# Performance work log

Hardware: AMD Instinct MI355X
Metric: run time of the kernel (lower is better)

## Reference

```python
import jax, jax.numpy as jnp
import numpy as np

N, D_IN, D_OUT, H = 8192, 512, 512, 8


def setup_inputs() -> dict:
    key = jax.random.key(0)
    k1, k2, k3, k4, k5 = jax.random.split(key, 5)
    x = jax.random.normal(k1, (N, D_IN), dtype=jnp.float32)
    adj = jax.random.randint(k2, (N, N), 0, 2, dtype=jnp.int32)
    W = jax.random.normal(k3, (D_OUT, D_IN), dtype=jnp.float32) * (1.0 / np.sqrt(D_IN))
    b = jax.random.normal(k4, (D_OUT,), dtype=jnp.float32) * 0.01
    a = jax.random.normal(k5, (H, 2 * (D_OUT // H)), dtype=jnp.float32)
    return {"x": x, "adj": adj, "W": W, "b": b, "a": a}


def reference(x, adj, W, b, a):
    # h = Linear(x): torch Linear stores W as [out, in]
    h = x @ W.T + b  # [N, D_OUT]
    # NOTE: the original forward computes dense GAT attention scores,
    # a masked softmax over adj, and an attention-weighted aggregation,
    # but then discards all of it and returns self.act(h). That attention
    # path is dead code (no effect on the output), so the faithful forward
    # is exactly GELU(Wx + b). torch.nn.GELU default is the exact erf form.
    return jax.nn.gelu(h, approximate=False)
```

## Files before the change

kernel.cpp:

```cpp
#include <hip/hip_runtime.h>
#include <hip/hip_bf16.h>
#include <math.h>


#define NROWS 8192
#define KD    512
#define NOUT  512

using short8  = __attribute__((ext_vector_type(8))) short;
using floatx4 = __attribute__((ext_vector_type(4))) float;

#define GLOBAL_AS(p) ((const __attribute__((address_space(1))) void*)(p))
#define LDS_AS(p)    ((__attribute__((address_space(3))) void*)(p))

__device__ __forceinline__ unsigned short f32_to_bf16(float f) {
  unsigned int u = __float_as_uint(f);
  u += 0x7FFFu + ((u >> 16) & 1u);
  return (unsigned short)(u >> 16);
}

__global__ __launch_bounds__(256) void cast_bf16_kernel(
    const float* __restrict__ x, const float* __restrict__ W,
    unsigned short* __restrict__ xb, unsigned short* __restrict__ wb) {
  const int i  = blockIdx.x * 256 + threadIdx.x;
  const int XV = (NROWS * KD) / 8;
  const float* src;
  unsigned short* dst;
  int idx;
  if (i < XV) { src = x; dst = xb; idx = i; }
  else        { src = W; dst = wb; idx = i - XV; }
  floatx4 v0 = ((const floatx4*)src)[idx * 2 + 0];
  floatx4 v1 = ((const floatx4*)src)[idx * 2 + 1];
  short8 o;
  o[0] = (short)f32_to_bf16(v0[0]);
  o[1] = (short)f32_to_bf16(v0[1]);
  o[2] = (short)f32_to_bf16(v0[2]);
  o[3] = (short)f32_to_bf16(v0[3]);
  o[4] = (short)f32_to_bf16(v1[0]);
  o[5] = (short)f32_to_bf16(v1[1]);
  o[6] = (short)f32_to_bf16(v1[2]);
  o[7] = (short)f32_to_bf16(v1[3]);
  *(short8*)(dst + (size_t)idx * 8) = o;
}

__global__ __launch_bounds__(256) void gemm_bias_gelu(
    const unsigned short* __restrict__ A,
    const unsigned short* __restrict__ B,
    const float* __restrict__ bias,
    float* __restrict__ C) {
  __shared__ __align__(16) unsigned short lA[128 * 32];
  __shared__ __align__(16) unsigned short lB[128 * 32];

  const int tid  = threadIdx.x;
  const int bn   = blockIdx.x;
  const int bm   = blockIdx.y;
  const int wave = tid >> 6;
  const int lane = tid & 63;
  const int quad = lane >> 4;
  const int l16  = lane & 15;
  const int wm   = (wave >> 1) * 64;
  const int wn   = (wave & 1) * 64;

  const int r0 = tid >> 2;
  const int e0 = (tid & 3) * 8;
  unsigned short* lA0 = lA + wave * 512;
  unsigned short* lA1 = lA + 2048 + wave * 512;
  unsigned short* lB0 = lB + wave * 512;
  unsigned short* lB1 = lB + 2048 + wave * 512;

  const unsigned short* Ab = A + (size_t)bm * 128 * KD;
  const unsigned short* Bb = B + (size_t)bn * 128 * KD;

  floatx4 acc[4][4] = {};

  for (int kt = 0; kt < KD / 32; ++kt) {
    const int k0 = kt * 32;
    const unsigned short* ga0 = Ab + (size_t)r0 * KD + k0 + e0;
    const unsigned short* ga1 = ga0 + (size_t)64 * KD;
    const unsigned short* gb0 = Bb + (size_t)r0 * KD + k0 + e0;
    const unsigned short* gb1 = gb0 + (size_t)64 * KD;

    __builtin_amdgcn_global_load_lds(GLOBAL_AS(ga0), LDS_AS(lA0), 16, 0, 0);
    __builtin_amdgcn_global_load_lds(GLOBAL_AS(ga1), LDS_AS(lA1), 16, 0, 0);
    __builtin_amdgcn_global_load_lds(GLOBAL_AS(gb0), LDS_AS(lB0), 16, 0, 0);
    __builtin_amdgcn_global_load_lds(GLOBAL_AS(gb1), LDS_AS(lB1), 16, 0, 0);
    __syncthreads();

    short8 af[4], bfr[4];
#pragma unroll
    for (int t = 0; t < 4; ++t) {
      af[t]  = *(const short8*)(lA + (wm + t * 16 + l16) * 32 + quad * 8);
      bfr[t] = *(const short8*)(lB + (wn + t * 16 + l16) * 32 + quad * 8);
    }
#pragma unroll
    for (int i = 0; i < 4; ++i)
#pragma unroll
      for (int j = 0; j < 4; ++j)
        acc[i][j] =
            __builtin_amdgcn_mfma_f32_16x16x32_bf16(af[i], bfr[j], acc[i][j], 0, 0, 0);
    __syncthreads();
  }

  const int row0 = bm * 128 + wm;
  const int col0 = bn * 128 + wn;
#pragma unroll
  for (int i = 0; i < 4; ++i) {
#pragma unroll
    for (int j = 0; j < 4; ++j) {
      const int col = col0 + j * 16 + l16;
      const float bv = bias[col];
#pragma unroll
      for (int r = 0; r < 4; ++r) {
        const int row = row0 + i * 16 + quad * 4 + r;
        float v = acc[i][j][r] + bv;
        float g = 0.5f * v * (1.0f + erff(v * 0.70710678118654752f));
        C[(size_t)row * NOUT + col] = g;
      }
    }
  }
}

extern "C" void kernel_launch(void* const* d_in, const int* in_sizes, int n_in,
                              void* d_out, int out_size, void* d_ws, size_t ws_size,
                              hipStream_t stream) {
  const float* x = (const float*)d_in[0];
  const float* W = (const float*)d_in[2];
  const float* b = (const float*)d_in[3];
  float* out = (float*)d_out;

  unsigned short* xb = (unsigned short*)d_ws;
  unsigned short* wb = xb + (size_t)NROWS * KD;

  cast_bf16_kernel<<<dim3(2176), dim3(256), 0, stream>>>(x, W, xb, wb);
  gemm_bias_gelu<<<dim3(4, 64), dim3(256), 0, stream>>>(xb, wb, b, out);
}
```

Baseline: 334.6 us.

## Fuse bf16 cast into GEMM with register-prefetched double-buffered LDS tiles

Removes the separate fp32-to-bf16 cast kernel and its workspace round trip. The GEMM now loads fp32 x and W directly, converts them to bf16 in registers and writes them into double-buffered LDS, prefetching the next K tile while computing the current one. This drops one barrier per iteration. The tile shrinks to 64x128 to give 512 blocks at occupancy 2. In exchange, W is re-read and re-converted by every row block, and rounding is now round-half-up instead of round-to-nearest-even.

```diff
diff --git a/kernel.cpp b/kernel.cpp
--- a/kernel.cpp
+++ b/kernel.cpp
@@ -1,120 +1,112 @@
 #include <hip/hip_runtime.h>
-#include <hip/hip_bf16.h>
 #include <math.h>
 
 
-#define NROWS 8192
-#define KD    512
-#define NOUT  512
+#define KD   512
+#define BM   64
+#define BN   128
+#define BK   32
 
 using short8  = __attribute__((ext_vector_type(8))) short;
 using floatx4 = __attribute__((ext_vector_type(4))) float;
+using uintx4  = __attribute__((ext_vector_type(4))) unsigned int;
 
-#define GLOBAL_AS(p) ((const __attribute__((address_space(1))) void*)(p))
-#define LDS_AS(p)    ((__attribute__((address_space(3))) void*)(p))
-
-__device__ __forceinline__ unsigned short f32_to_bf16(float f) {
-  unsigned int u = __float_as_uint(f);
-  u += 0x7FFFu + ((u >> 16) & 1u);
-  return (unsigned short)(u >> 16);
+__device__ __forceinline__ unsigned int pack2_bf16(float lo, float hi) {
+  unsigned int ul = __float_as_uint(lo) + 0x8000u;
+  unsigned int uh = __float_as_uint(hi) + 0x8000u;
+  return __builtin_amdgcn_perm(uh, ul, 0x07060302u);
 }
 
-__global__ __launch_bounds__(256) void cast_bf16_kernel(
-    const float* __restrict__ x, const float* __restrict__ W,
-    unsigned short* __restrict__ xb, unsigned short* __restrict__ wb) {
-  const int i  = blockIdx.x * 256 + threadIdx.x;
-  const int XV = (NROWS * KD) / 8;
-  const float* src;
-  unsigned short* dst;
-  int idx;
-  if (i < XV) { src = x; dst = xb; idx = i; }
-  else        { src = W; dst = wb; idx = i - XV; }
-  floatx4 v0 = ((const floatx4*)src)[idx * 2 + 0];
-  floatx4 v1 = ((const floatx4*)src)[idx * 2 + 1];
-  short8 o;
-  o[0] = (short)f32_to_bf16(v0[0]);
-  o[1] = (short)f32_to_bf16(v0[1]);
-  o[2] = (short)f32_to_bf16(v0[2]);
-  o[3] = (short)f32_to_bf16(v0[3]);
-  o[4] = (short)f32_to_bf16(v1[0]);
-  o[5] = (short)f32_to_bf16(v1[1]);
-  o[6] = (short)f32_to_bf16(v1[2]);
-  o[7] = (short)f32_to_bf16(v1[3]);
-  *(short8*)(dst + (size_t)idx * 8) = o;
+__device__ __forceinline__ uintx4 pack8_bf16(floatx4 v0, floatx4 v1) {
+  uintx4 o;
+  o[0] = pack2_bf16(v0[0], v0[1]);
+  o[1] = pack2_bf16(v0[2], v0[3]);
+  o[2] = pack2_bf16(v1[0], v1[1]);
+  o[3] = pack2_bf16(v1[2], v1[3]);
+  return o;
 }
 
-__global__ __launch_bounds__(256) void gemm_bias_gelu(
-    const unsigned short* __restrict__ A,
-    const unsigned short* __restrict__ B,
+__global__ __launch_bounds__(256, 2) void fused_gemm_bias_gelu(
+    const float* __restrict__ X,
+    const float* __restrict__ W,
     const float* __restrict__ bias,
     float* __restrict__ C) {
-  __shared__ __align__(16) unsigned short lA[128 * 32];
-  __shared__ __align__(16) unsigned short lB[128 * 32];
+  __shared__ __align__(16) unsigned short lA[2][BM * BK];
+  __shared__ __align__(16) unsigned short lB[2][BN * BK];
 
   const int tid  = threadIdx.x;
-  const int bn   = blockIdx.x;
-  const int bm   = blockIdx.y;
+  const int id   = blockIdx.x;
+  const int bm   = id & 127;
+  const int bn   = id >> 7;
   const int wave = tid >> 6;
   const int lane = tid & 63;
   const int quad = lane >> 4;
   const int l16  = lane & 15;
-  const int wm   = (wave >> 1) * 64;
+  const int wm   = (wave >> 1) * 32;
   const int wn   = (wave & 1) * 64;
 
-  const int r0 = tid >> 2;
-  const int e0 = (tid & 3) * 8;
-  unsigned short* lA0 = lA + wave * 512;
-  unsigned short* lA1 = lA + 2048 + wave * 512;
-  unsigned short* lB0 = lB + wave * 512;
-  unsigned short* lB1 = lB + 2048 + wave * 512;
+  const int rA = tid >> 2, eA = (tid & 3) * 8;
+  const int rB = tid >> 1, eB = (tid & 1) * 16;
 
-  const unsigned short* Ab = A + (size_t)bm * 128 * KD;
-  const unsigned short* Bb = B + (size_t)bn * 128 * KD;
+  const float* Ag = X + (size_t)(bm * BM + rA) * KD + eA;
+  const float* Bg = W + (size_t)(bn * BN + rB) * KD + eB;
 
-  floatx4 acc[4][4] = {};
+  floatx4 a0, a1, b0, b1, b2, b3;
+#define ISSUE_LOADS(kt)                                  \
+  do {                                                   \
+    const float* pa = Ag + (kt) * BK;                    \
+    a0 = *(const floatx4*)pa;                            \
+    a1 = *(const floatx4*)(pa + 4);                      \
+    const float* pb = Bg + (kt) * BK;                    \
+    b0 = *(const floatx4*)pb;                            \
+    b1 = *(const floatx4*)(pb + 4);                      \
+    b2 = *(const floatx4*)(pb + 8);                      \
+    b3 = *(const floatx4*)(pb + 12);                     \
+  } while (0)
 
-  for (int kt = 0; kt < KD / 32; ++kt) {
-    const int k0 = kt * 32;
-    const unsigned short* ga0 = Ab + (size_t)r0 * KD + k0 + e0;
-    const unsigned short* ga1 = ga0 + (size_t)64 * KD;
-    const unsigned short* gb0 = Bb + (size_t)r0 * KD + k0 + e0;
-    const unsigned short* gb1 = gb0 + (size_t)64 * KD;
+  ISSUE_LOADS(0);
+  floatx4 acc[2][4] = {};
 
-    __builtin_amdgcn_global_load_lds(GLOBAL_AS(ga0), LDS_AS(lA0), 16, 0, 0);
-    __builtin_amdgcn_global_load_lds(GLOBAL_AS(ga1), LDS_AS(lA1), 16, 0, 0);
-    __builtin_amdgcn_global_load_lds(GLOBAL_AS(gb0), LDS_AS(lB0), 16, 0, 0);
-    __builtin_amdgcn_global_load_lds(GLOBAL_AS(gb1), LDS_AS(lB1), 16, 0, 0);
+#pragma unroll
+  for (int kt = 0; kt < KD / BK; ++kt) {
+    const int buf = kt & 1;
+    *(uintx4*)&lA[buf][rA * BK + eA]      = pack8_bf16(a0, a1);
+    *(uintx4*)&lB[buf][rB * BK + eB]      = pack8_bf16(b0, b1);
+    *(uintx4*)&lB[buf][rB * BK + eB + 8]  = pack8_bf16(b2, b3);
+    if (kt < KD / BK - 1) ISSUE_LOADS(kt + 1);
     __syncthreads();
-
-    short8 af[4], bfr[4];
+    short8 af[2], bfr[4];
 #pragma unroll
-    for (int t = 0; t < 4; ++t) {
-      af[t]  = *(const short8*)(lA + (wm + t * 16 + l16) * 32 + quad * 8);
-      bfr[t] = *(const short8*)(lB + (wn + t * 16 + l16) * 32 + quad * 8);
-    }
+    for (int i = 0; i < 2; ++i)
+      af[i] = *(const short8*)&lA[buf][(wm + i * 16 + l16) * BK + quad * 8];
 #pragma unroll
-    for (int i = 0; i < 4; ++i)
+    for (int j = 0; j < 4; ++j)
+      bfr[j] = *(const short8*)&lB[buf][(wn + j * 16 + l16) * BK + quad * 8];
+#pragma unroll
+    for (int i = 0; i < 2; ++i)
 #pragma unroll
       for (int j = 0; j < 4; ++j)
-        acc[i][j] =
-            __builtin_amdgcn_mfma_f32_16x16x32_bf16(af[i], bfr[j], acc[i][j], 0, 0, 0);
-    __syncthreads();
+        acc[i][j] = __builtin_amdgcn_mfma_f32_16x16x32_bf16(af[i], bfr[j],
+                                                            acc[i][j], 0, 0, 0);
   }
+#undef ISSUE_LOADS
 
-  const int row0 = bm * 128 + wm;
-  const int col0 = bn * 128 + wn;
+  const int row0 = bm * BM + wm;
+  const int col0 = bn * BN + wn;
+  float bv[4];
 #pragma unroll
-  for (int i = 0; i < 4; ++i) {
+  for (int j = 0; j < 4; ++j) bv[j] = bias[col0 + j * 16 + l16];
+#pragma unroll
+  for (int i = 0; i < 2; ++i) {
 #pragma unroll
     for (int j = 0; j < 4; ++j) {
       const int col = col0 + j * 16 + l16;
-      const float bv = bias[col];
 #pragma unroll
       for (int r = 0; r < 4; ++r) {
         const int row = row0 + i * 16 + quad * 4 + r;
-        float v = acc[i][j][r] + bv;
+        float v = acc[i][j][r] + bv[j];
         float g = 0.5f * v * (1.0f + erff(v * 0.70710678118654752f));
-        C[(size_t)row * NOUT + col] = g;
+        C[(size_t)row * KD + col] = g;
       }
     }
   }
@@ -127,10 +119,5 @@
   const float* W = (const float*)d_in[2];
   const float* b = (const float*)d_in[3];
   float* out = (float*)d_out;
-
-  unsigned short* xb = (unsigned short*)d_ws;
-  unsigned short* wb = xb + (size_t)NROWS * KD;
-
-  cast_bf16_kernel<<<dim3(2176), dim3(256), 0, stream>>>(x, W, xb, wb);
-  gemm_bias_gelu<<<dim3(4, 64), dim3(256), 0, stream>>>(xb, wb, b, out);
+  fused_gemm_bias_gelu<<<dim3(512), dim3(256), 0, stream>>>(x, W, b, out);
 }
```

Result: no change. 329.4 us (-1.5%).
